# Kernel optimization log

Measured on AMD Instinct MI355X. Metric: run time of the kernel, lower is better.

The kernel has to match this reference:

```python
import jax, jax.numpy as jnp
import numpy as np

N = 50000   # nodes
E = 800000  # edges (before self-loops)
B = 2       # extra batch dim
EPS = 1e-5  # BatchNorm eps


def _glorot(k, fi, fo):
    return jax.random.normal(k, (fi, fo), jnp.float32) * (1.0 / np.sqrt(fi))


def setup_inputs() -> dict:
    key = jax.random.key(0)
    ks = jax.random.split(key, 8)
    x = jax.random.normal(ks[0], (1, B, N, 216), jnp.float32)
    edge_index = jax.random.randint(ks[1], (2, E), 0, N, dtype=jnp.int64)
    return {
        "x": x,
        "W1": _glorot(ks[2], 216, 64), "b1": jnp.zeros((64,), jnp.float32),
        "g1": jnp.ones((64,), jnp.float32), "be1": jnp.zeros((64,), jnp.float32),
        "W2": _glorot(ks[3], 64, 8), "b2": jnp.zeros((8,), jnp.float32),
        "g2": jnp.ones((8,), jnp.float32), "be2": jnp.zeros((8,), jnp.float32),
        "W3": _glorot(ks[4], 8, 3), "b3": jnp.zeros((3,), jnp.float32),
        "edge_index": edge_index,
    }


def _gcn_norm(edge_index, n):
    # add self-loops, symmetric normalization D^-1/2 (A+I) D^-1/2
    loops = jnp.arange(n, dtype=edge_index.dtype)
    row = jnp.concatenate([edge_index[0], loops])
    col = jnp.concatenate([edge_index[1], loops])
    deg = jnp.zeros((n,), jnp.float32).at[col].add(1.0)
    dinv = jnp.where(deg > 0, jax.lax.rsqrt(deg), 0.0)
    norm = dinv[row] * dinv[col]  # [E+N]
    return row, col, norm


def _gcn(x, W, b, row, col, norm):
    # x: [1, B, N, Fin]; transform then propagate along node axis (-2)
    xw = jnp.einsum('ubnf,fo->ubno', x, W)
    msgs = xw[:, :, row, :] * norm[None, None, :, None]     # gather at sources
    out = jnp.zeros_like(xw).at[:, :, col, :].add(msgs)     # scatter to targets
    return out + b


def _bn(h, g, be):
    # h: [B, C, N]; batch statistics over (B, N) per channel (training mode)
    mean = h.mean(axis=(0, 2), keepdims=True)
    var = h.var(axis=(0, 2), keepdims=True)
    return (h - mean) * jax.lax.rsqrt(var + EPS) * g[None, :, None] + be[None, :, None]


def reference(x, W1, b1, g1, be1, W2, b2, g2, be2, W3, b3, edge_index):
    n = x.shape[-2]
    row, col, norm = _gcn_norm(edge_index, n)

    h = jax.nn.relu(_gcn(x, W1, b1, row, col, norm))        # [1,B,N,64]
    h = jnp.swapaxes(h[0], 1, 2)                            # [B,64,N]
    h = _bn(h, g1, be1)
    h = jnp.swapaxes(h, 1, 2)[None]                         # [1,B,N,64]

    x1 = _gcn(h, W2, b2, row, col, norm)                    # [1,B,N,8]
    x2 = jax.nn.relu(x1)
    x2 = jnp.swapaxes(x2[0], 1, 2)                          # [B,8,N]
    x2 = _bn(x2, g2, be2)
    x2 = jnp.swapaxes(x2, 1, 2)[None]                       # [1,B,N,8]

    out = _gcn(x2, W3, b3, row, col, norm)                  # [1,B,N,3]
    return (out, x1)
```

## Files before the change

kernel.cpp:

```cpp
#include <hip/hip_runtime.h>
#include <stdint.h>

#define N_NODES 50000
#define N_EDGES 800000
#define BB 2
#define F0 216
#define ROWS (BB*N_NODES)
#define BN_EPS 1e-5f
#define NSB 49


__global__ void k_count(const int* __restrict__ ei, int* __restrict__ cnt) {
    int e = blockIdx.x*blockDim.x + threadIdx.x;
    if (e < N_EDGES) {
        int c = ei[N_EDGES + e];
        atomicAdd(&cnt[c], 1);
    }
}

__global__ void k_dinv(const int* __restrict__ cnt, float* __restrict__ dinv) {
    int i = blockIdx.x*blockDim.x + threadIdx.x;
    if (i < N_NODES) dinv[i] = rsqrtf((float)(cnt[i] + 1));
}

__global__ void k_scanA(const int* __restrict__ cnt, int* __restrict__ incl, int* __restrict__ part) {
    __shared__ int s[1024];
    int t = threadIdx.x;
    int i = blockIdx.x*1024 + t;
    s[t] = (i < N_NODES) ? cnt[i] : 0;
    __syncthreads();
    for (int off=1; off<1024; off<<=1) {
        int a = (t >= off) ? s[t-off] : 0;
        __syncthreads();
        s[t] += a;
        __syncthreads();
    }
    if (i < N_NODES) incl[i] = s[t];
    if (t == 1023) part[blockIdx.x] = s[t];
}

__global__ void k_scanB(int* part) {
    if (threadIdx.x == 0 && blockIdx.x == 0) {
        int run = 0;
        for (int b=0; b<NSB; b++) { int v = part[b]; part[b] = run; run += v; }
    }
}

__global__ void k_scanC(const int* __restrict__ cnt, const int* __restrict__ incl, const int* __restrict__ part,
                        int* __restrict__ offs, int* __restrict__ cursor) {
    int i = blockIdx.x*1024 + threadIdx.x;
    if (i < N_NODES) {
        int inc = part[blockIdx.x] + incl[i];
        int ex = inc - cnt[i];
        offs[i] = ex; cursor[i] = ex;
        if (i == N_NODES-1) offs[N_NODES] = inc;
    }
}

__global__ void k_fill(const int* __restrict__ ei, const float* __restrict__ dinv,
                       int* __restrict__ cursor, int* __restrict__ csr_src, float* __restrict__ csr_w) {
    int e = blockIdx.x*blockDim.x + threadIdx.x;
    if (e < N_EDGES) {
        int r = ei[e];
        int c = ei[N_EDGES + e];
        int slot = atomicAdd(&cursor[c], 1);
        csr_src[slot] = r;
        csr_w[slot]  = dinv[r];
    }
}

__global__ __launch_bounds__(256) void k_gemm1(const float* __restrict__ x, const float* __restrict__ W1,
                                               float* __restrict__ xw) {
    __shared__ float xs[64*F0];
    int t = threadIdx.x;
    int row0 = blockIdx.x * 64;
    int validFloats = (ROWS - row0) * F0;
    const float4* xg = reinterpret_cast<const float4*>(x + (size_t)row0 * F0);
    float4* xs4 = reinterpret_cast<float4*>(xs);
    float4 z; z.x=z.y=z.z=z.w=0.f;
    for (int idx = t; idx < (64*F0)/4; idx += 256)
        xs4[idx] = (idx*4 < validFloats) ? xg[idx] : z;
    __syncthreads();

    int o2 = t & 31;
    int rg = t >> 5;
    float accA[8], accB[8];
    #pragma unroll
    for (int j=0;j<8;j++){ accA[j]=0.f; accB[j]=0.f; }
    const float4* xv = reinterpret_cast<const float4*>(xs + rg*8*F0);
    for (int k4=0; k4<F0/4; k4++) {
        float wA[4], wB[4];
        #pragma unroll
        for (int i=0;i<4;i++){
            wA[i] = W1[(4*k4+i)*64 + o2];
            wB[i] = W1[(4*k4+i)*64 + o2 + 32];
        }
        #pragma unroll
        for (int j=0;j<8;j++) {
            float4 xj = xv[j*(F0/4) + k4];
            accA[j] += xj.x*wA[0] + xj.y*wA[1] + xj.z*wA[2] + xj.w*wA[3];
            accB[j] += xj.x*wB[0] + xj.y*wB[1] + xj.z*wB[2] + xj.w*wB[3];
        }
    }
    #pragma unroll
    for (int j=0;j<8;j++) {
        int grow = row0 + rg*8 + j;
        if (grow < ROWS) {
            xw[(size_t)grow*64 + o2]      = accA[j];
            xw[(size_t)grow*64 + o2 + 32] = accB[j];
        }
    }
}

__global__ __launch_bounds__(256) void k_prop1(const float* __restrict__ xw, const int* __restrict__ offs,
                       const int* __restrict__ csr_src, const float* __restrict__ csr_w,
                       const float* __restrict__ dinv, const float* __restrict__ b1,
                       float* __restrict__ h, float* __restrict__ stat) {
    __shared__ float lsum[64], lsq[64];
    int t = threadIdx.x;
    if (t < 64) { lsum[t]=0.f; lsq[t]=0.f; }
    __syncthreads();
    int f = t & 63;
    int wid = blockIdx.x*4 + (t>>6);
    int nwaves = gridDim.x*4;
    float bias = b1[f];
    float ls=0.f, lq=0.f;
    for (int d = wid; d < N_NODES; d += nwaves) {
        int s0 = offs[d], s1 = offs[d+1];
        float a0=0.f, a1=0.f;
        for (int e=s0; e<s1; e++) {
            int src = csr_src[e];
            float w = csr_w[e];
            a0 += w * xw[(size_t)src*64 + f];
            a1 += w * xw[(size_t)(N_NODES+src)*64 + f];
        }
        float sd = dinv[d];
        a0 += sd * xw[(size_t)d*64 + f];
        a1 += sd * xw[(size_t)(N_NODES+d)*64 + f];
        float h0 = fmaxf(sd*a0 + bias, 0.f);
        float h1 = fmaxf(sd*a1 + bias, 0.f);
        h[(size_t)d*64 + f] = h0;
        h[(size_t)(N_NODES+d)*64 + f] = h1;
        ls += h0 + h1;
        lq += h0*h0 + h1*h1;
    }
    atomicAdd(&lsum[f], ls);
    atomicAdd(&lsq[f], lq);
    __syncthreads();
    if (t < 64) {
        atomicAdd(&stat[t],     lsum[t]);
        atomicAdd(&stat[64+t],  lsq[t]);
    }
}

__global__ void k_bnfin(const float* __restrict__ stat, const float* __restrict__ g,
                        const float* __restrict__ be, float* __restrict__ sc, int C) {
    int f = threadIdx.x;
    if (f < C) {
        float inv_n = 1.0f / (float)(BB*N_NODES);
        float mean = stat[f]*inv_n;
        float var  = stat[C+f]*inv_n - mean*mean;
        float is   = rsqrtf(var + BN_EPS);
        float scale = g[f]*is;
        sc[f]   = scale;
        sc[C+f] = be[f] - mean*scale;
    }
}

__global__ __launch_bounds__(256) void k_bn1_gemm2(const float* __restrict__ h, const float* __restrict__ sc1,
                        const float* __restrict__ W2, float* __restrict__ t2) {
    __shared__ float hs[32][68];
    __shared__ float w2s[64*8];
    int t = threadIdx.x;
    for (int i=t; i<512; i+=256) w2s[i] = W2[i];
    int row0 = blockIdx.x*32;
    for (int idx=t; idx<2048; idx+=256) {
        int r = idx>>6, f = idx&63;
        int grow = row0 + r;
        hs[r][f] = (grow < ROWS) ? h[(size_t)grow*64+f]*sc1[f] + sc1[64+f] : 0.f;
    }
    __syncthreads();
    int r = t >> 3, o = t & 7;
    float acc = 0.f;
    #pragma unroll
    for (int f=0; f<64; f++) acc += hs[r][f] * w2s[f*8+o];
    int grow = row0 + r;
    if (grow < ROWS) t2[(size_t)grow*8 + o] = acc;
}

__global__ __launch_bounds__(256) void k_prop2(const float* __restrict__ t2, const int* __restrict__ offs,
                       const int* __restrict__ csr_src, const float* __restrict__ csr_w,
                       const float* __restrict__ dinv, const float* __restrict__ b2,
                       float* __restrict__ x1_out, float* __restrict__ stat) {
    __shared__ float lsum[8], lsq[8];
    int t = threadIdx.x;
    if (t < 8) { lsum[t]=0.f; lsq[t]=0.f; }
    __syncthreads();
    int lane = t & 63;
    int o = lane & 7, b = (lane>>3)&1, es = lane>>4;
    int wid = blockIdx.x*4 + (t>>6);
    int nwaves = gridDim.x*4;
    float bias = b2[o];
    float ls=0.f, lq=0.f;
    for (int d=wid; d<N_NODES; d+=nwaves) {
        int s0=offs[d], s1=offs[d+1];
        float acc=0.f;
        for (int e=s0+es; e<s1; e+=4) {
            acc += csr_w[e] * t2[(size_t)(b*N_NODES+csr_src[e])*8 + o];
        }
        acc += __shfl_xor(acc, 16, 64);
        acc += __shfl_xor(acc, 32, 64);
        float sd = dinv[d];
        float val = sd*(acc + sd*t2[(size_t)(b*N_NODES+d)*8 + o]) + bias;
        if (es == 0) {
            x1_out[(size_t)(b*N_NODES+d)*8 + o] = val;
            float rv = fmaxf(val, 0.f);
            ls += rv; lq += rv*rv;
        }
    }
    if (es == 0) { atomicAdd(&lsum[o], ls); atomicAdd(&lsq[o], lq); }
    __syncthreads();
    if (t < 8) { atomicAdd(&stat[t], lsum[t]); atomicAdd(&stat[8+t], lsq[t]); }
}

__global__ void k_bn2_gemm3(const float* __restrict__ x1, const float* __restrict__ sc2,
                            const float* __restrict__ W3, float* __restrict__ t3) {
    int rowi = blockIdx.x*blockDim.x + threadIdx.x;
    if (rowi < ROWS) {
        float v[8];
        #pragma unroll
        for (int o=0;o<8;o++) {
            float r = fmaxf(x1[(size_t)rowi*8+o], 0.f);
            v[o] = r*sc2[o] + sc2[8+o];
        }
        #pragma unroll
        for (int c=0;c<3;c++) {
            float acc=0.f;
            #pragma unroll
            for (int o=0;o<8;o++) acc += v[o]*W3[o*3+c];
            t3[(size_t)rowi*4+c] = acc;
        }
        t3[(size_t)rowi*4+3] = 0.f;
    }
}

__global__ __launch_bounds__(256) void k_prop3(const float* __restrict__ t3, const int* __restrict__ offs,
                       const int* __restrict__ csr_src, const float* __restrict__ csr_w,
                       const float* __restrict__ dinv, const float* __restrict__ b3,
                       float* __restrict__ outp) {
    int t = threadIdx.x;
    int lane = t & 63;
    int c = lane & 3, b = (lane>>2)&1, es = lane>>3;
    int wid = blockIdx.x*4 + (t>>6);
    int nwaves = gridDim.x*4;
    float bias = (c<3) ? b3[c] : 0.f;
    for (int d=wid; d<N_NODES; d+=nwaves) {
        int s0=offs[d], s1=offs[d+1];
        float acc=0.f;
        for (int e=s0+es; e<s1; e+=8) {
            acc += csr_w[e] * t3[(size_t)(b*N_NODES+csr_src[e])*4 + c];
        }
        acc += __shfl_xor(acc, 8, 64);
        acc += __shfl_xor(acc, 16, 64);
        acc += __shfl_xor(acc, 32, 64);
        float sd = dinv[d];
        float val = sd*(acc + sd*t3[(size_t)(b*N_NODES+d)*4 + c]) + bias;
        if (es == 0 && c < 3) outp[(size_t)(b*N_NODES+d)*3 + c] = val;
    }
}

static inline size_t align256(size_t x){ return (x + 255) & ~(size_t)255; }

extern "C" void kernel_launch(void* const* d_in, const int* in_sizes, int n_in,
                              void* d_out, int out_size, void* d_ws, size_t ws_size,
                              hipStream_t stream) {
    const float* x   = (const float*)d_in[0];
    const float* W1  = (const float*)d_in[1];
    const float* b1  = (const float*)d_in[2];
    const float* g1  = (const float*)d_in[3];
    const float* be1 = (const float*)d_in[4];
    const float* W2  = (const float*)d_in[5];
    const float* b2  = (const float*)d_in[6];
    const float* g2  = (const float*)d_in[7];
    const float* be2 = (const float*)d_in[8];
    const float* W3  = (const float*)d_in[9];
    const float* b3  = (const float*)d_in[10];
    const int*   ei  = (const int*)d_in[11];

    float* outp   = (float*)d_out;
    float* x1_out = (float*)d_out + BB*N_NODES*3;

    char* w = (char*)d_ws;
    size_t off = 0;
    auto alloc = [&](size_t bytes) { void* p = w + off; off = align256(off + bytes); return p; };
    int*   cnt    = (int*)  alloc(N_NODES*4);
    float* stat1  = (float*)alloc(128*4);
    float* stat2  = (float*)alloc(16*4);
    size_t zero_bytes = off;
    float* dinv   = (float*)alloc(N_NODES*4);
    int*   incl   = (int*)  alloc(N_NODES*4);
    int*   part   = (int*)  alloc(64*4);
    int*   offs   = (int*)  alloc((N_NODES+1)*4);
    int*   cursor = (int*)  alloc(N_NODES*4);
    int*   csr_src= (int*)  alloc((size_t)N_EDGES*4);
    float* csr_w  = (float*)alloc((size_t)N_EDGES*4);
    float* xw     = (float*)alloc((size_t)ROWS*64*4);
    float* h      = (float*)alloc((size_t)ROWS*64*4);
    float* sc1    = (float*)alloc(128*4);
    float* sc2    = (float*)alloc(16*4);
    float* t2     = xw;
    float* t3     = h;
    (void)ws_size; (void)in_sizes; (void)n_in; (void)out_size;

    hipMemsetAsync(d_ws, 0, zero_bytes, stream);

    k_count <<<(N_EDGES+255)/256, 256, 0, stream>>>(ei, cnt);
    k_dinv  <<<(N_NODES+255)/256, 256, 0, stream>>>(cnt, dinv);
    k_scanA <<<NSB, 1024, 0, stream>>>(cnt, incl, part);
    k_scanB <<<1, 64, 0, stream>>>(part);
    k_scanC <<<NSB, 1024, 0, stream>>>(cnt, incl, part, offs, cursor);
    k_fill  <<<(N_EDGES+255)/256, 256, 0, stream>>>(ei, dinv, cursor, csr_src, csr_w);

    k_gemm1 <<<(ROWS+63)/64, 256, 0, stream>>>(x, W1, xw);
    k_prop1 <<<1024, 256, 0, stream>>>(xw, offs, csr_src, csr_w, dinv, b1, h, stat1);
    k_bnfin <<<1, 64, 0, stream>>>(stat1, g1, be1, sc1, 64);
    k_bn1_gemm2 <<<(ROWS+31)/32, 256, 0, stream>>>(h, sc1, W2, t2);
    k_prop2 <<<1024, 256, 0, stream>>>(t2, offs, csr_src, csr_w, dinv, b2, x1_out, stat2);
    k_bnfin <<<1, 64, 0, stream>>>(stat2, g2, be2, sc2, 8);
    k_bn2_gemm3 <<<(ROWS+255)/256, 256, 0, stream>>>(x1_out, sc2, W3, t3);
    k_prop3 <<<1024, 256, 0, stream>>>(t3, offs, csr_src, csr_w, dinv, b3, outp);
}
```

Measured before the change: 591.4 us.

## Transpose gemm1 tile in LDS, unroll propagation loops, double prop grid sizes

k_gemm1 now stores the input tile k-major in shared memory and loads W1 in chunks of 24 into registers, so each thread reads eight consecutive rows as float4 broadcasts. It also sets launch_bounds to allow two blocks per CU. The propagation kernels use multiple independent accumulators to expose more memory-level parallelism in the gather loops. Their grids are doubled from 1024 to 2048 blocks. The register arrays raise register pressure, the transposed LDS writes may cause bank conflicts, and the separate accumulators change floating-point summation order slightly.

```diff
diff --git a/kernel.cpp b/kernel.cpp
--- a/kernel.cpp
+++ b/kernel.cpp
@@ -69,45 +69,62 @@
     }
 }
 
-__global__ __launch_bounds__(256) void k_gemm1(const float* __restrict__ x, const float* __restrict__ W1,
-                                               float* __restrict__ xw) {
-    __shared__ float xs[64*F0];
+#define KC 24
+__global__ __launch_bounds__(256,2) void k_gemm1(const float* __restrict__ x, const float* __restrict__ W1,
+                                                 float* __restrict__ xw) {
+    __shared__ float xs[F0*64];
     int t = threadIdx.x;
     int row0 = blockIdx.x * 64;
-    int validFloats = (ROWS - row0) * F0;
-    const float4* xg = reinterpret_cast<const float4*>(x + (size_t)row0 * F0);
-    float4* xs4 = reinterpret_cast<float4*>(xs);
-    float4 z; z.x=z.y=z.z=z.w=0.f;
-    for (int idx = t; idx < (64*F0)/4; idx += 256)
-        xs4[idx] = (idx*4 < validFloats) ? xg[idx] : z;
+
+    int r  = t & 63;
+    int kg = t >> 6;
+    bool rowok = (row0 + r) < ROWS;
+    const float* xr = x + (size_t)(row0 + r) * F0;
+    for (int kb = 0; kb < F0; kb += 16) {
+        int k0 = kb + kg*4;
+        if (k0 < F0) {
+            float4 v; v.x=v.y=v.z=v.w=0.f;
+            if (rowok) v = *reinterpret_cast<const float4*>(xr + k0);
+            xs[(k0+0)*64 + r] = v.x;
+            xs[(k0+1)*64 + r] = v.y;
+            xs[(k0+2)*64 + r] = v.z;
+            xs[(k0+3)*64 + r] = v.w;
+        }
+    }
     __syncthreads();
 
     int o2 = t & 31;
     int rg = t >> 5;
-    float accA[8], accB[8];
+    float acc0[8], acc1[8];
     #pragma unroll
-    for (int j=0;j<8;j++){ accA[j]=0.f; accB[j]=0.f; }
-    const float4* xv = reinterpret_cast<const float4*>(xs + rg*8*F0);
-    for (int k4=0; k4<F0/4; k4++) {
-        float wA[4], wB[4];
+    for (int j=0;j<8;j++){ acc0[j]=0.f; acc1[j]=0.f; }
+
+    for (int kc = 0; kc < F0; kc += KC) {
+        float wa[KC], wb[KC];
         #pragma unroll
-        for (int i=0;i<4;i++){
-            wA[i] = W1[(4*k4+i)*64 + o2];
-            wB[i] = W1[(4*k4+i)*64 + o2 + 32];
+        for (int kk=0; kk<KC; kk++) {
+            wa[kk] = W1[(kc+kk)*64 + o2];
+            wb[kk] = W1[(kc+kk)*64 + o2 + 32];
         }
         #pragma unroll
-        for (int j=0;j<8;j++) {
-            float4 xj = xv[j*(F0/4) + k4];
-            accA[j] += xj.x*wA[0] + xj.y*wA[1] + xj.z*wA[2] + xj.w*wA[3];
-            accB[j] += xj.x*wB[0] + xj.y*wB[1] + xj.z*wB[2] + xj.w*wB[3];
-        }
-    }
+        for (int kk=0; kk<KC; kk++) {
+            const float* xk = xs + (kc+kk)*64 + rg*8;
+            float4 x0 = *reinterpret_cast<const float4*>(xk);
+            float4 x1 = *reinterpret_cast<const float4*>(xk + 4);
+            float w0 = wa[kk], w1 = wb[kk];
+            acc0[0] += x0.x*w0; acc0[1] += x0.y*w0; acc0[2] += x0.z*w0; acc0[3] += x0.w*w0;
+            acc0[4] += x1.x*w0; acc0[5] += x1.y*w0; acc0[6] += x1.z*w0; acc0[7] += x1.w*w0;
+            acc1[0] += x0.x*w1; acc1[1] += x0.y*w1; acc1[2] += x0.z*w1; acc1[3] += x0.w*w1;
+            acc1[4] += x1.x*w1; acc1[5] += x1.y*w1; acc1[6] += x1.z*w1; acc1[7] += x1.w*w1;
+        }
+    }
+
     #pragma unroll
     for (int j=0;j<8;j++) {
         int grow = row0 + rg*8 + j;
         if (grow < ROWS) {
-            xw[(size_t)grow*64 + o2]      = accA[j];
-            xw[(size_t)grow*64 + o2 + 32] = accB[j];
+            xw[(size_t)grow*64 + o2]      = acc0[j];
+            xw[(size_t)grow*64 + o2 + 32] = acc1[j];
         }
     }
 }
@@ -127,13 +144,22 @@
     float ls=0.f, lq=0.f;
     for (int d = wid; d < N_NODES; d += nwaves) {
         int s0 = offs[d], s1 = offs[d+1];
-        float a0=0.f, a1=0.f;
-        for (int e=s0; e<s1; e++) {
-            int src = csr_src[e];
-            float w = csr_w[e];
-            a0 += w * xw[(size_t)src*64 + f];
-            a1 += w * xw[(size_t)(N_NODES+src)*64 + f];
-        }
+        float a0=0.f, a1=0.f, p0=0.f, p1=0.f, q0=0.f, q1=0.f, r0=0.f, r1=0.f;
+        int e = s0;
+        for (; e+4 <= s1; e += 4) {
+            int i0=csr_src[e], i1=csr_src[e+1], i2=csr_src[e+2], i3=csr_src[e+3];
+            float w0=csr_w[e], w1=csr_w[e+1], w2=csr_w[e+2], w3=csr_w[e+3];
+            a0 += w0*xw[(size_t)i0*64+f];  a1 += w0*xw[(size_t)(N_NODES+i0)*64+f];
+            p0 += w1*xw[(size_t)i1*64+f];  p1 += w1*xw[(size_t)(N_NODES+i1)*64+f];
+            q0 += w2*xw[(size_t)i2*64+f];  q1 += w2*xw[(size_t)(N_NODES+i2)*64+f];
+            r0 += w3*xw[(size_t)i3*64+f];  r1 += w3*xw[(size_t)(N_NODES+i3)*64+f];
+        }
+        for (; e < s1; e++) {
+            int src = csr_src[e]; float w = csr_w[e];
+            a0 += w*xw[(size_t)src*64+f];  a1 += w*xw[(size_t)(N_NODES+src)*64+f];
+        }
+        a0 += p0 + q0 + r0;
+        a1 += p1 + q1 + r1;
         float sd = dinv[d];
         a0 += sd * xw[(size_t)d*64 + f];
         a1 += sd * xw[(size_t)(N_NODES+d)*64 + f];
@@ -204,10 +230,14 @@
     float ls=0.f, lq=0.f;
     for (int d=wid; d<N_NODES; d+=nwaves) {
         int s0=offs[d], s1=offs[d+1];
-        float acc=0.f;
-        for (int e=s0+es; e<s1; e+=4) {
-            acc += csr_w[e] * t2[(size_t)(b*N_NODES+csr_src[e])*8 + o];
-        }
+        float accA=0.f, accB=0.f;
+        int e = s0 + es;
+        for (; e+4 < s1; e += 8) {
+            accA += csr_w[e]   * t2[(size_t)(b*N_NODES+csr_src[e])*8 + o];
+            accB += csr_w[e+4] * t2[(size_t)(b*N_NODES+csr_src[e+4])*8 + o];
+        }
+        if (e < s1) accA += csr_w[e] * t2[(size_t)(b*N_NODES+csr_src[e])*8 + o];
+        float acc = accA + accB;
         acc += __shfl_xor(acc, 16, 64);
         acc += __shfl_xor(acc, 32, 64);
         float sd = dinv[d];
@@ -256,10 +286,14 @@
     float bias = (c<3) ? b3[c] : 0.f;
     for (int d=wid; d<N_NODES; d+=nwaves) {
         int s0=offs[d], s1=offs[d+1];
-        float acc=0.f;
-        for (int e=s0+es; e<s1; e+=8) {
-            acc += csr_w[e] * t3[(size_t)(b*N_NODES+csr_src[e])*4 + c];
-        }
+        float accA=0.f, accB=0.f;
+        int e = s0 + es;
+        for (; e+8 < s1; e += 16) {
+            accA += csr_w[e]   * t3[(size_t)(b*N_NODES+csr_src[e])*4 + c];
+            accB += csr_w[e+8] * t3[(size_t)(b*N_NODES+csr_src[e+8])*4 + c];
+        }
+        if (e < s1) accA += csr_w[e] * t3[(size_t)(b*N_NODES+csr_src[e])*4 + c];
+        float acc = accA + accB;
         acc += __shfl_xor(acc, 8, 64);
         acc += __shfl_xor(acc, 16, 64);
         acc += __shfl_xor(acc, 32, 64);
@@ -322,11 +356,11 @@
     k_fill  <<<(N_EDGES+255)/256, 256, 0, stream>>>(ei, dinv, cursor, csr_src, csr_w);
 
     k_gemm1 <<<(ROWS+63)/64, 256, 0, stream>>>(x, W1, xw);
-    k_prop1 <<<1024, 256, 0, stream>>>(xw, offs, csr_src, csr_w, dinv, b1, h, stat1);
+    k_prop1 <<<2048, 256, 0, stream>>>(xw, offs, csr_src, csr_w, dinv, b1, h, stat1);
     k_bnfin <<<1, 64, 0, stream>>>(stat1, g1, be1, sc1, 64);
     k_bn1_gemm2 <<<(ROWS+31)/32, 256, 0, stream>>>(h, sc1, W2, t2);
-    k_prop2 <<<1024, 256, 0, stream>>>(t2, offs, csr_src, csr_w, dinv, b2, x1_out, stat2);
+    k_prop2 <<<2048, 256, 0, stream>>>(t2, offs, csr_src, csr_w, dinv, b2, x1_out, stat2);
     k_bnfin <<<1, 64, 0, stream>>>(stat2, g2, be2, sc2, 8);
     k_bn2_gemm3 <<<(ROWS+255)/256, 256, 0, stream>>>(x1_out, sc2, W3, t3);
-    k_prop3 <<<1024, 256, 0, stream>>>(t3, offs, csr_src, csr_w, dinv, b3, outp);
-}
+    k_prop3 <<<2048, 256, 0, stream>>>(t3, offs, csr_src, csr_w, dinv, b3, outp);
+}
```

Measured after the change: 514.5 us. -13.0%, faster.
